# Optimization experiments

Measured on AMD Instinct MI355X. Metric: run time of the kernel, lower is better.

Reference implementation:

```python
import jax, jax.numpy as jnp
import numpy as np

EPS = 1e-5
N_NODES = 50000


def batchnorm(x, gamma, beta):
    # training-mode BatchNorm1d: batch mean, biased variance
    mean = jnp.mean(x, axis=0)
    var = jnp.mean(jnp.square(x - mean), axis=0)
    return (x - mean) * jax.lax.rsqrt(var + EPS) * gamma + beta


def setup_inputs() -> dict:
    key = jax.random.key(0)
    ks = jax.random.split(key, 8)
    N, E, D_IN, D_H, D_OUT = N_NODES, 800000, 128, 128, 128
    feat = jax.random.normal(ks[0], (N, D_IN), dtype=jnp.float32)
    w = jax.random.uniform(ks[1], (E,), dtype=jnp.float32)
    # xavier_uniform with relu gain for Q and W
    gain = float(np.sqrt(2.0))
    bq = gain * np.sqrt(6.0 / (D_IN + D_H))
    bw = gain * np.sqrt(6.0 / (D_IN + D_H + D_OUT))
    Q_w = jax.random.uniform(ks[2], (D_H, D_IN), minval=-bq, maxval=bq, dtype=jnp.float32)
    W_w = jax.random.uniform(ks[3], (D_OUT, D_IN + D_H), minval=-bw, maxval=bw, dtype=jnp.float32)
    Q_b = jnp.zeros((D_H,), jnp.float32)
    W_b = jnp.zeros((D_OUT,), jnp.float32)
    gamma2 = jnp.ones((D_OUT,), jnp.float32)
    beta2 = jnp.zeros((D_OUT,), jnp.float32)
    src = jax.random.randint(ks[4], (E,), 0, N, dtype=jnp.int32)
    dst = jax.random.randint(ks[5], (E,), 0, N, dtype=jnp.int32)
    return {"feat": feat, "w": w, "Q_w": Q_w, "Q_b": Q_b, "W_w": W_w,
            "W_b": W_b, "gamma2": gamma2, "beta2": beta2, "src": src, "dst": dst}


def reference(feat, w, Q_w, Q_b, W_w, W_b, gamma2, beta2, src, dst):
    N = feat.shape[0]
    # h = dropout(bnorm_two(relu(Q(feat))))  (dropout=0 -> identity; source reuses bnorm_two)
    h = batchnorm(jax.nn.relu(feat @ Q_w.T + Q_b), gamma2, beta2)  # [N, H]
    # weighted neighbor mean: sum_e w_e * h[src_e] scattered to dst, / sum_e w_e
    num = jax.ops.segment_sum(w[:, None] * h[src], dst, num_segments=N)  # [N, H]
    den = jax.ops.segment_sum(w, dst, num_segments=N)  # [N]
    has_msg = den[:, None] != 0
    agg = jnp.where(has_msg, num / jnp.where(has_msg, den[:, None], 1.0), h)
    rst = jnp.concatenate([feat, agg], axis=1) @ W_w.T + W_b  # [N, OUT]
    rst = batchnorm(jax.nn.relu(rst), gamma2, beta2)
    denom = jnp.linalg.norm(rst, axis=1, keepdims=True)
    return rst / jnp.where(denom == 0, 1.0, denom)
```

## Files before the change

### kernel.cpp

```cpp
#include <hip/hip_runtime.h>
#include <stdint.h>


#define BN_EPS 1e-5f
#define NSLOT 32

typedef __attribute__((ext_vector_type(8))) short bf16x8;
typedef __attribute__((ext_vector_type(4))) float f32x4;

static __device__ __forceinline__ unsigned short f2bf(float f) {
    uint32_t u = __builtin_bit_cast(uint32_t, f);
    u += 0x7fffu + ((u >> 16) & 1u);
    return (unsigned short)(u >> 16);
}
static __device__ __forceinline__ float bf_lo(uint32_t u) {
    return __builtin_bit_cast(float, u << 16);
}
static __device__ __forceinline__ float bf_hi(uint32_t u) {
    return __builtin_bit_cast(float, u & 0xffff0000u);
}

__global__ __launch_bounds__(256) void k_pre(
    const float* __restrict__ feat, unsigned short* __restrict__ featb, int nf,
    const int* __restrict__ dst, int* __restrict__ ccnt, int E, int CB)
{
    if ((int)blockIdx.x < CB) {
        int i = (blockIdx.x * 256 + threadIdx.x) * 4;
        if (i + 3 < nf) {
            float4 v = *(const float4*)(feat + i);
            ushort4 o;
            o.x = f2bf(v.x); o.y = f2bf(v.y); o.z = f2bf(v.z); o.w = f2bf(v.w);
            *(ushort4*)(featb + i) = o;
        } else {
            for (int j = i; j < nf; ++j) featb[j] = f2bf(feat[j]);
        }
    } else {
        __shared__ int hcnt[128];
        const int tid = threadIdx.x;
        if (tid < 128) hcnt[tid] = 0;
        __syncthreads();
        const int base_e = (blockIdx.x - CB) * 2048;
#pragma unroll
        for (int j = 0; j < 8; ++j) {
            int e = base_e + j * 256 + tid;
            if (e < E) atomicAdd(&hcnt[dst[e] >> 9], 1);
        }
        __syncthreads();
        if (tid < 128 && hcnt[tid] > 0) atomicAdd(&ccnt[tid], hcnt[tid]);
    }
}

__global__ __launch_bounds__(128) void k_coffs(
    const int* __restrict__ ccnt, int* __restrict__ coffs,
    int* __restrict__ gcur, int* __restrict__ offs, int N, int E)
{
    __shared__ int w0sum;
    const int t = threadIdx.x;
    const int lane = t & 63, wv = t >> 6;
    int v = ccnt[t];
    int incl = v;
#pragma unroll
    for (int o = 1; o < 64; o <<= 1) {
        int u = __shfl_up(incl, o, 64);
        if (lane >= o) incl += u;
    }
    if (wv == 0 && lane == 63) w0sum = incl;
    __syncthreads();
    int excl = incl - v + (wv ? w0sum : 0);
    coffs[t] = excl;
    gcur[t]  = excl;
    if (t == 127) { coffs[128] = excl + v; offs[N] = E; }
}

template<int K>
__global__ __launch_bounds__(256) void gemm_bn(
    const unsigned short* __restrict__ A_lo,
    const unsigned short* __restrict__ A_hi,
    const float* __restrict__ B,
    const float* __restrict__ bias,
    float* __restrict__ Y,
    double* __restrict__ sum, double* __restrict__ sumsq, int N)
{
    constexpr int SA = 72;
    __shared__ unsigned short As[64 * SA];
    __shared__ unsigned short Bs[128 * SA];
    __shared__ float bsum_s[128], bsq_s[128];

    const int tid  = threadIdx.x;
    const int lane = tid & 63;
    const int wv   = tid >> 6;
    const int wr   = wv >> 1;
    const int wc   = wv & 1;
    const int m15  = lane & 15;
    const int quad = lane >> 4;
    const int r0   = blockIdx.x * 64;

    if (tid < 128) { bsum_s[tid] = 0.f; bsq_s[tid] = 0.f; }

    f32x4 acc[2][4];
#pragma unroll
    for (int rt = 0; rt < 2; ++rt)
#pragma unroll
        for (int ct = 0; ct < 4; ++ct)
            acc[rt][ct] = (f32x4){0.f, 0.f, 0.f, 0.f};

    for (int kc = 0; kc < K; kc += 64) {
        const unsigned short* Ap = (kc < 128) ? A_lo : A_hi;
        const int koff = kc & 127;
#pragma unroll
        for (int i = 0; i < 2; ++i) {
            int idx = i * 256 + tid;
            int row = idx >> 3, seg = idx & 7;
            int gr  = r0 + row; if (gr >= N) gr = N - 1;
            uint4 v = *(const uint4*)(Ap + (size_t)gr * 128 + koff + seg * 8);
            *(uint4*)(As + row * SA + seg * 8) = v;
        }
#pragma unroll
        for (int i = 0; i < 8; ++i) {
            int idx = i * 256 + tid;
            int row = idx >> 4, seg = idx & 15;
            float4 v = *(const float4*)(B + (size_t)row * K + kc + seg * 4);
            ushort4 o;
            o.x = f2bf(v.x); o.y = f2bf(v.y); o.z = f2bf(v.z); o.w = f2bf(v.w);
            *(ushort4*)(Bs + row * SA + seg * 4) = o;
        }
        __syncthreads();

#pragma unroll
        for (int ks = 0; ks < 64; ks += 32) {
            bf16x8 af[2], bfr[4];
#pragma unroll
            for (int rt = 0; rt < 2; ++rt)
                af[rt] = *(const bf16x8*)(As + (wr * 32 + rt * 16 + m15) * SA + ks + quad * 8);
#pragma unroll
            for (int ct = 0; ct < 4; ++ct)
                bfr[ct] = *(const bf16x8*)(Bs + (wc * 64 + ct * 16 + m15) * SA + ks + quad * 8);
#pragma unroll
            for (int rt = 0; rt < 2; ++rt)
#pragma unroll
                for (int ct = 0; ct < 4; ++ct)
                    acc[rt][ct] = __builtin_amdgcn_mfma_f32_16x16x32_bf16(
                        af[rt], bfr[ct], acc[rt][ct], 0, 0, 0);
        }
        __syncthreads();
    }

#pragma unroll
    for (int ct = 0; ct < 4; ++ct) {
        int col = wc * 64 + ct * 16 + m15;
        float bz = bias[col];
        float s = 0.f, q = 0.f;
#pragma unroll
        for (int rt = 0; rt < 2; ++rt) {
#pragma unroll
            for (int reg = 0; reg < 4; ++reg) {
                int row = r0 + wr * 32 + rt * 16 + quad * 4 + reg;
                float v = fmaxf(acc[rt][ct][reg] + bz, 0.f);
                if (row < N) {
                    Y[(size_t)row * 128 + col] = v;
                } else {
                    v = 0.f;
                }
                s += v; q = fmaf(v, v, q);
            }
        }
        s += __shfl_xor(s, 16, 64); s += __shfl_xor(s, 32, 64);
        q += __shfl_xor(q, 16, 64); q += __shfl_xor(q, 32, 64);
        if (quad == 0) {
            atomicAdd(&bsum_s[col], s);
            atomicAdd(&bsq_s[col], q);
        }
    }
    __syncthreads();
    if (tid < 128) {
        const int slot = (blockIdx.x & (NSLOT - 1)) * 128;
        atomicAdd(&sum[slot + tid],   (double)bsum_s[tid]);
        atomicAdd(&sumsq[slot + tid], (double)bsq_s[tid]);
    }
}

__global__ __launch_bounds__(128) void bn_coef(
    const double* __restrict__ sum, const double* __restrict__ sumsq,
    const float* __restrict__ gamma, const float* __restrict__ beta,
    float* __restrict__ a, float* __restrict__ b, double invN)
{
    const int t = threadIdx.x;
    double ms = 0.0, qs = 0.0;
#pragma unroll
    for (int s = 0; s < NSLOT; ++s) {
        ms += sum[s * 128 + t];
        qs += sumsq[s * 128 + t];
    }
    float mean = (float)(ms * invN);
    float var  = (float)(qs * invN) - mean * mean;
    float sc = rsqrtf(var + BN_EPS) * gamma[t];
    a[t] = sc;
    b[t] = fmaf(-mean, sc, beta[t]);
}

__global__ __launch_bounds__(256) void apply_bn_bf16(
    const float* __restrict__ y,
    const float* __restrict__ a, const float* __restrict__ b,
    unsigned short* __restrict__ h, int n)
{
    int i = (blockIdx.x * 256 + threadIdx.x) * 4;
    if (i >= n) return;
    int c = i & 127;
    float4 v  = *(const float4*)(y + i);
    float4 av = *(const float4*)(a + c);
    float4 bv = *(const float4*)(b + c);
    ushort4 o;
    o.x = f2bf(fmaf(av.x, v.x, bv.x));
    o.y = f2bf(fmaf(av.y, v.y, bv.y));
    o.z = f2bf(fmaf(av.z, v.z, bv.z));
    o.w = f2bf(fmaf(av.w, v.w, bv.w));
    *(ushort4*)(h + i) = o;
}

__global__ __launch_bounds__(256) void k_bin(
    const int* __restrict__ src, const int* __restrict__ dst,
    const float* __restrict__ w, int* __restrict__ gcur,
    int4* __restrict__ tmp, int E)
{
    __shared__ int hcnt[128];
    __shared__ int hbase[128];
    const int tid = threadIdx.x;
    if (tid < 128) hcnt[tid] = 0;
    __syncthreads();

    int d8[8], s8[8], slot8[8];
    float w8[8];
#pragma unroll
    for (int j = 0; j < 8; ++j) {
        int e = blockIdx.x * 2048 + j * 256 + tid;
        if (e < E) {
            d8[j] = dst[e]; s8[j] = src[e]; w8[j] = w[e];
            slot8[j] = atomicAdd(&hcnt[d8[j] >> 9], 1);
        } else d8[j] = -1;
    }
    __syncthreads();
    if (tid < 128 && hcnt[tid] > 0)
        hbase[tid] = atomicAdd(&gcur[tid], hcnt[tid]);
    __syncthreads();
#pragma unroll
    for (int j = 0; j < 8; ++j) {
        if (d8[j] >= 0) {
            int pos = hbase[d8[j] >> 9] + slot8[j];
            tmp[pos] = make_int4(s8[j], __float_as_int(w8[j]), d8[j], 0);
        }
    }
}

__global__ __launch_bounds__(256) void k_refine(
    const int4* __restrict__ tmp, const int* __restrict__ coffs,
    int* __restrict__ offs, int2* __restrict__ epack, int N)
{
    __shared__ int hist[512];
    __shared__ int wpre[4];
    const int b    = blockIdx.x;
    const int d0   = b << 9;
    const int dlim = min(512, N - d0);
    const int tid  = threadIdx.x;
    const int lane = tid & 63, wv = tid >> 6;
    const int start = coffs[b];
    const int end   = coffs[b + 1];

    hist[tid] = 0; hist[tid + 256] = 0;
    __syncthreads();

    for (int p = start + tid; p < end; p += 256)
        atomicAdd(&hist[tmp[p].z - d0], 1);
    __syncthreads();

    int v0 = hist[2 * tid], v1 = hist[2 * tid + 1];
    int s = v0 + v1;
    int incl = s;
#pragma unroll
    for (int o = 1; o < 64; o <<= 1) {
        int t = __shfl_up(incl, o, 64);
        if (lane >= o) incl += t;
    }
    if (lane == 63) wpre[wv] = incl;
    __syncthreads();
    if (tid == 0) {
        int r = 0;
#pragma unroll
        for (int i = 0; i < 4; ++i) { int t = wpre[i]; wpre[i] = r; r += t; }
    }
    __syncthreads();
    int e0 = start + wpre[wv] + incl - s;
    if (2 * tid < dlim)     offs[d0 + 2 * tid]     = e0;
    if (2 * tid + 1 < dlim) offs[d0 + 2 * tid + 1] = e0 + v0;
    hist[2 * tid]     = e0;
    hist[2 * tid + 1] = e0 + v0;
    __syncthreads();

    for (int p = start + tid; p < end; p += 256) {
        int4 rec = tmp[p];
        int pos = atomicAdd(&hist[rec.z - d0], 1);
        epack[pos] = make_int2(rec.x, rec.y);
    }
}

__global__ __launch_bounds__(256) void gather_agg(
    const unsigned short* __restrict__ h,
    const int* __restrict__ offs, const int2* __restrict__ epack,
    unsigned short* __restrict__ aggb, int N)
{
    const int r    = (int)((blockIdx.x * 256u + threadIdx.x) >> 6);
    const int lane = threadIdx.x & 63;
    if (r >= N) return;
    int p = offs[r];
    const int end = offs[r + 1];
    float nx = 0.f, ny = 0.f, den = 0.f;
    for (; p + 3 < end; p += 4) {
        int2 e0 = epack[p],     e1 = epack[p + 1];
        int2 e2 = epack[p + 2], e3 = epack[p + 3];
        uint32_t u0 = *(const uint32_t*)(h + (size_t)e0.x * 128 + 2 * lane);
        uint32_t u1 = *(const uint32_t*)(h + (size_t)e1.x * 128 + 2 * lane);
        uint32_t u2 = *(const uint32_t*)(h + (size_t)e2.x * 128 + 2 * lane);
        uint32_t u3 = *(const uint32_t*)(h + (size_t)e3.x * 128 + 2 * lane);
        float w0 = __int_as_float(e0.y), w1 = __int_as_float(e1.y);
        float w2 = __int_as_float(e2.y), w3 = __int_as_float(e3.y);
        nx = fmaf(w0, bf_lo(u0), nx); ny = fmaf(w0, bf_hi(u0), ny);
        nx = fmaf(w1, bf_lo(u1), nx); ny = fmaf(w1, bf_hi(u1), ny);
        nx = fmaf(w2, bf_lo(u2), nx); ny = fmaf(w2, bf_hi(u2), ny);
        nx = fmaf(w3, bf_lo(u3), nx); ny = fmaf(w3, bf_hi(u3), ny);
        den += (w0 + w1) + (w2 + w3);
    }
    for (; p < end; ++p) {
        int2 e0 = epack[p];
        float w0 = __int_as_float(e0.y);
        uint32_t u0 = *(const uint32_t*)(h + (size_t)e0.x * 128 + 2 * lane);
        nx = fmaf(w0, bf_lo(u0), nx); ny = fmaf(w0, bf_hi(u0), ny);
        den += w0;
    }
    float2 outv;
    if (den != 0.f) {
        float inv = 1.f / den;
        outv.x = nx * inv; outv.y = ny * inv;
    } else {
        uint32_t u = *(const uint32_t*)(h + (size_t)r * 128 + 2 * lane);
        outv.x = bf_lo(u); outv.y = bf_hi(u);
    }
    ushort2 ao; ao.x = f2bf(outv.x); ao.y = f2bf(outv.y);
    *(ushort2*)&aggb[(size_t)r * 128 + 2 * lane] = ao;
}

__global__ __launch_bounds__(256) void finalize(
    const float* __restrict__ Y2,
    const float* __restrict__ a, const float* __restrict__ b,
    float* __restrict__ out, int N)
{
    __shared__ float sa[128], sb[128];
    const int t = threadIdx.x;
    if (t < 128) { sa[t] = a[t]; sb[t] = b[t]; }
    __syncthreads();
    const int row  = (int)((blockIdx.x * 256u + t) >> 6);
    const int lane = t & 63;
    if (row >= N) return;
    const size_t base = (size_t)row * 128;
    float v0 = fmaf(sa[lane],      Y2[base + lane],      sb[lane]);
    float v1 = fmaf(sa[lane + 64], Y2[base + lane + 64], sb[lane + 64]);
    float ss = fmaf(v0, v0, v1 * v1);
#pragma unroll
    for (int o = 32; o; o >>= 1) ss += __shfl_xor(ss, o, 64);
    float nrm = sqrtf(ss);
    float inv = (nrm == 0.f) ? 1.f : 1.f / nrm;
    out[base + lane]      = v0 * inv;
    out[base + lane + 64] = v1 * inv;
}

extern "C" void kernel_launch(void* const* d_in, const int* in_sizes, int n_in,
                              void* d_out, int out_size, void* d_ws, size_t ws_size,
                              hipStream_t stream)
{
    const float* feat   = (const float*)d_in[0];
    const float* w      = (const float*)d_in[1];
    const float* Q_w    = (const float*)d_in[2];
    const float* Q_b    = (const float*)d_in[3];
    const float* W_w    = (const float*)d_in[4];
    const float* W_b    = (const float*)d_in[5];
    const float* gamma2 = (const float*)d_in[6];
    const float* beta2  = (const float*)d_in[7];
    const int*   src    = (const int*)d_in[8];
    const int*   dst    = (const int*)d_in[9];

    const int N = in_sizes[0] / 128;
    const int E = in_sizes[1];

    float*          y1    = (float*)d_ws;
    unsigned short* featb = (unsigned short*)(y1 + (size_t)N * 128);
    unsigned short* aggb  = featb + (size_t)N * 128;
    unsigned short* h_bf  = aggb + (size_t)N * 128;
    int4*  tmp    = (int4*)(h_bf + (size_t)N * 128);
    int2*  epack  = (int2*)(tmp + E);
    int*   offs   = (int*)(epack + E);
    int*   coffs  = offs + (N + 1);
    int*   gcur   = coffs + 129;
    float* coefs  = (float*)(gcur + 128);
    float* a1 = coefs, *b1 = coefs + 128, *a2 = coefs + 256, *b2 = coefs + 384;
    uintptr_t sp  = ((uintptr_t)(coefs + 512) + 7) & ~(uintptr_t)7;
    double* stats = (double*)sp;
    double* sum1   = stats;
    double* sumsq1 = stats + NSLOT * 128;
    double* sum2   = stats + 2 * NSLOT * 128;
    double* sumsq2 = stats + 3 * NSLOT * 128;
    int*   ccnt   = (int*)(stats + 4 * NSLOT * 128);

    hipMemsetAsync(stats, 0,
                   4 * NSLOT * 128 * sizeof(double) + 128 * sizeof(int),
                   stream);

    const double invN = 1.0 / (double)N;
    const int gemm_blocks = (N + 63) / 64;
    const int NB = (N + 511) >> 9;
    const int CB = (N * 128 / 4 + 255) / 256;
    const int HB = (E + 2047) / 2048;

    k_pre<<<CB + HB, 256, 0, stream>>>(feat, featb, N * 128, dst, ccnt, E, CB);
    k_coffs<<<1, 128, 0, stream>>>(ccnt, coffs, gcur, offs, N, E);

    k_bin<<<HB, 256, 0, stream>>>(src, dst, w, gcur, tmp, E);
    k_refine<<<NB, 256, 0, stream>>>(tmp, coffs, offs, epack, N);

    gemm_bn<128><<<gemm_blocks, 256, 0, stream>>>(
        featb, featb, Q_w, Q_b, y1, sum1, sumsq1, N);
    bn_coef<<<1, 128, 0, stream>>>(sum1, sumsq1, gamma2, beta2, a1, b1, invN);
    apply_bn_bf16<<<(N * 128 + 1023) / 1024, 256, 0, stream>>>(
        y1, a1, b1, h_bf, N * 128);

    gather_agg<<<(N * 64 + 255) / 256, 256, 0, stream>>>(h_bf, offs, epack, aggb, N);

    gemm_bn<256><<<gemm_blocks, 256, 0, stream>>>(
        featb, aggb, W_w, W_b, y1 , sum2, sumsq2, N);
    bn_coef<<<1, 128, 0, stream>>>(sum2, sumsq2, gamma2, beta2, a2, b2, invN);
    finalize<<<(N * 64 + 255) / 256, 256, 0, stream>>>(
        y1, a2, b2, (float*)d_out, N);
}
```

Measured before the change: 254.3 us.

## Merge independent kernels into combined launches via block-index dispatch

Combines edge binning and the first GEMM+BN-stat pass into one launch, with blocks split by index range. It also combines CSR refinement with the BN-apply-to-bf16 pass. This removes two kernel launches and lets independent graph-preprocessing work run alongside dense work on the same device. The cost is that the union of shared memory and register use from both bodies now applies to every block, which may reduce occupancy.

```diff
diff --git a/kernel.cpp b/kernel.cpp
--- a/kernel.cpp
+++ b/kernel.cpp
@@ -73,7 +73,8 @@
 }
 
 template<int K>
-__global__ __launch_bounds__(256) void gemm_bn(
+static __device__ __forceinline__ void gemm_body(
+    int bid,
     const unsigned short* __restrict__ A_lo,
     const unsigned short* __restrict__ A_hi,
     const float* __restrict__ B,
@@ -93,7 +94,7 @@
     const int wc   = wv & 1;
     const int m15  = lane & 15;
     const int quad = lane >> 4;
-    const int r0   = blockIdx.x * 64;
+    const int r0   = bid * 64;
 
     if (tid < 128) { bsum_s[tid] = 0.f; bsq_s[tid] = 0.f; }
 
@@ -173,10 +174,60 @@
     }
     __syncthreads();
     if (tid < 128) {
-        const int slot = (blockIdx.x & (NSLOT - 1)) * 128;
+        const int slot = (bid & (NSLOT - 1)) * 128;
         atomicAdd(&sum[slot + tid],   (double)bsum_s[tid]);
         atomicAdd(&sumsq[slot + tid], (double)bsq_s[tid]);
     }
+}
+
+static __device__ __forceinline__ void bin_body(
+    int bid,
+    const int* __restrict__ src, const int* __restrict__ dst,
+    const float* __restrict__ w, int* __restrict__ gcur,
+    int4* __restrict__ tmp, int E)
+{
+    __shared__ int hcnt[128];
+    __shared__ int hbase[128];
+    const int tid = threadIdx.x;
+    if (tid < 128) hcnt[tid] = 0;
+    __syncthreads();
+
+    int d8[8], s8[8], slot8[8];
+    float w8[8];
+#pragma unroll
+    for (int j = 0; j < 8; ++j) {
+        int e = bid * 2048 + j * 256 + tid;
+        if (e < E) {
+            d8[j] = dst[e]; s8[j] = src[e]; w8[j] = w[e];
+            slot8[j] = atomicAdd(&hcnt[d8[j] >> 9], 1);
+        } else d8[j] = -1;
+    }
+    __syncthreads();
+    if (tid < 128 && hcnt[tid] > 0)
+        hbase[tid] = atomicAdd(&gcur[tid], hcnt[tid]);
+    __syncthreads();
+#pragma unroll
+    for (int j = 0; j < 8; ++j) {
+        if (d8[j] >= 0) {
+            int pos = hbase[d8[j] >> 9] + slot8[j];
+            tmp[pos] = make_int4(s8[j], __float_as_int(w8[j]), d8[j], 0);
+        }
+    }
+}
+
+__global__ __launch_bounds__(256) void k_bin_gemm(
+    const int* __restrict__ src, const int* __restrict__ dst,
+    const float* __restrict__ w, int* __restrict__ gcur,
+    int4* __restrict__ tmp, int E, int HB,
+    const unsigned short* __restrict__ featb,
+    const float* __restrict__ Qw, const float* __restrict__ Qb,
+    float* __restrict__ y1,
+    double* __restrict__ sum, double* __restrict__ sumsq, int N)
+{
+    if ((int)blockIdx.x < HB)
+        bin_body(blockIdx.x, src, dst, w, gcur, tmp, E);
+    else
+        gemm_body<128>(blockIdx.x - HB, featb, featb, Qw, Qb, y1, sum, sumsq, N);
 }
 
 __global__ __launch_bounds__(128) void bn_coef(
@@ -198,66 +249,13 @@
     b[t] = fmaf(-mean, sc, beta[t]);
 }
 
-__global__ __launch_bounds__(256) void apply_bn_bf16(
-    const float* __restrict__ y,
-    const float* __restrict__ a, const float* __restrict__ b,
-    unsigned short* __restrict__ h, int n)
-{
-    int i = (blockIdx.x * 256 + threadIdx.x) * 4;
-    if (i >= n) return;
-    int c = i & 127;
-    float4 v  = *(const float4*)(y + i);
-    float4 av = *(const float4*)(a + c);
-    float4 bv = *(const float4*)(b + c);
-    ushort4 o;
-    o.x = f2bf(fmaf(av.x, v.x, bv.x));
-    o.y = f2bf(fmaf(av.y, v.y, bv.y));
-    o.z = f2bf(fmaf(av.z, v.z, bv.z));
-    o.w = f2bf(fmaf(av.w, v.w, bv.w));
-    *(ushort4*)(h + i) = o;
-}
-
-__global__ __launch_bounds__(256) void k_bin(
-    const int* __restrict__ src, const int* __restrict__ dst,
-    const float* __restrict__ w, int* __restrict__ gcur,
-    int4* __restrict__ tmp, int E)
-{
-    __shared__ int hcnt[128];
-    __shared__ int hbase[128];
-    const int tid = threadIdx.x;
-    if (tid < 128) hcnt[tid] = 0;
-    __syncthreads();
-
-    int d8[8], s8[8], slot8[8];
-    float w8[8];
-#pragma unroll
-    for (int j = 0; j < 8; ++j) {
-        int e = blockIdx.x * 2048 + j * 256 + tid;
-        if (e < E) {
-            d8[j] = dst[e]; s8[j] = src[e]; w8[j] = w[e];
-            slot8[j] = atomicAdd(&hcnt[d8[j] >> 9], 1);
-        } else d8[j] = -1;
-    }
-    __syncthreads();
-    if (tid < 128 && hcnt[tid] > 0)
-        hbase[tid] = atomicAdd(&gcur[tid], hcnt[tid]);
-    __syncthreads();
-#pragma unroll
-    for (int j = 0; j < 8; ++j) {
-        if (d8[j] >= 0) {
-            int pos = hbase[d8[j] >> 9] + slot8[j];
-            tmp[pos] = make_int4(s8[j], __float_as_int(w8[j]), d8[j], 0);
-        }
-    }
-}
-
-__global__ __launch_bounds__(256) void k_refine(
+static __device__ __forceinline__ void refine_body(
+    int b,
     const int4* __restrict__ tmp, const int* __restrict__ coffs,
     int* __restrict__ offs, int2* __restrict__ epack, int N)
 {
     __shared__ int hist[512];
     __shared__ int wpre[4];
-    const int b    = blockIdx.x;
     const int d0   = b << 9;
     const int dlim = min(512, N - d0);
     const int tid  = threadIdx.x;
@@ -299,6 +297,31 @@
         int4 rec = tmp[p];
         int pos = atomicAdd(&hist[rec.z - d0], 1);
         epack[pos] = make_int2(rec.x, rec.y);
+    }
+}
+
+__global__ __launch_bounds__(256) void k_refine_apply(
+    const int4* __restrict__ tmp, const int* __restrict__ coffs,
+    int* __restrict__ offs, int2* __restrict__ epack, int N, int NB,
+    const float* __restrict__ y,
+    const float* __restrict__ a, const float* __restrict__ b,
+    unsigned short* __restrict__ h, int n)
+{
+    if ((int)blockIdx.x < NB) {
+        refine_body(blockIdx.x, tmp, coffs, offs, epack, N);
+    } else {
+        int i = ((blockIdx.x - NB) * 256 + threadIdx.x) * 4;
+        if (i >= n) return;
+        int c = i & 127;
+        float4 v  = *(const float4*)(y + i);
+        float4 av = *(const float4*)(a + c);
+        float4 bv = *(const float4*)(b + c);
+        ushort4 o;
+        o.x = f2bf(fmaf(av.x, v.x, bv.x));
+        o.y = f2bf(fmaf(av.y, v.y, bv.y));
+        o.z = f2bf(fmaf(av.z, v.z, bv.z));
+        o.w = f2bf(fmaf(av.w, v.w, bv.w));
+        *(ushort4*)(h + i) = o;
     }
 }
 
@@ -347,6 +370,17 @@
     *(ushort2*)&aggb[(size_t)r * 128 + 2 * lane] = ao;
 }
 
+__global__ __launch_bounds__(256) void gemm_bn2(
+    const unsigned short* __restrict__ A_lo,
+    const unsigned short* __restrict__ A_hi,
+    const float* __restrict__ B,
+    const float* __restrict__ bias,
+    float* __restrict__ Y,
+    double* __restrict__ sum, double* __restrict__ sumsq, int N)
+{
+    gemm_body<256>(blockIdx.x, A_lo, A_hi, B, bias, Y, sum, sumsq, N);
+}
+
 __global__ __launch_bounds__(256) void finalize(
     const float* __restrict__ Y2,
     const float* __restrict__ a, const float* __restrict__ b,
@@ -413,26 +447,27 @@
                    stream);
 
     const double invN = 1.0 / (double)N;
-    const int gemm_blocks = (N + 63) / 64;
+    const int GB = (N + 63) / 64;
     const int NB = (N + 511) >> 9;
     const int CB = (N * 128 / 4 + 255) / 256;
     const int HB = (E + 2047) / 2048;
+    const int AB = (N * 128 / 4 + 255) / 256;
 
     k_pre<<<CB + HB, 256, 0, stream>>>(feat, featb, N * 128, dst, ccnt, E, CB);
     k_coffs<<<1, 128, 0, stream>>>(ccnt, coffs, gcur, offs, N, E);
 
-    k_bin<<<HB, 256, 0, stream>>>(src, dst, w, gcur, tmp, E);
-    k_refine<<<NB, 256, 0, stream>>>(tmp, coffs, offs, epack, N);
-
-    gemm_bn<128><<<gemm_blocks, 256, 0, stream>>>(
-        featb, featb, Q_w, Q_b, y1, sum1, sumsq1, N);
+    k_bin_gemm<<<HB + GB, 256, 0, stream>>>(
+        src, dst, w, gcur, tmp, E, HB,
+        featb, Q_w, Q_b, y1, sum1, sumsq1, N);
     bn_coef<<<1, 128, 0, stream>>>(sum1, sumsq1, gamma2, beta2, a1, b1, invN);
-    apply_bn_bf16<<<(N * 128 + 1023) / 1024, 256, 0, stream>>>(
+
+    k_refine_apply<<<NB + AB, 256, 0, stream>>>(
+        tmp, coffs, offs, epack, N, NB,
         y1, a1, b1, h_bf, N * 128);
 
     gather_agg<<<(N * 64 + 255) / 256, 256, 0, stream>>>(h_bf, offs, epack, aggb, N);
 
-    gemm_bn<256><<<gemm_blocks, 256, 0, stream>>>(
+    gemm_bn2<<<GB, 256, 0, stream>>>(
         featb, aggb, W_w, W_b, y1 , sum2, sumsq2, N);
     bn_coef<<<1, 128, 0, stream>>>(sum2, sumsq2, gamma2, beta2, a2, b2, invN);
     finalize<<<(N * 64 + 255) / 256, 256, 0, stream>>>(
```

After: 245.3 us. -3.6%, faster.

## Fuse all stages into one persistent cooperative kernel with grid syncs

Applied to the files above, without the earlier changes.

Replaces the chain of about a dozen kernel launches and the memset with a single cooperative persistent kernel. Stages are separated by grid.sync(), blocks loop over work units, and shared memory is a union reused across stages. Independent stages are merged into the same phase: edge binning runs alongside the first GEMM, and the refine step alongside BN apply. This removes launch gaps and idle tails between stages. In exchange it adds grid-wide barrier costs, caps the grid at the occupancy-derived block count, and keeps a multi-kernel fallback.

```diff
diff --git a/kernel.cpp b/kernel.cpp
--- a/kernel.cpp
+++ b/kernel.cpp
@@ -1,5 +1,8 @@
 #include <hip/hip_runtime.h>
+#include <hip/hip_cooperative_groups.h>
 #include <stdint.h>
+
+namespace cg = cooperative_groups;
 
 
 #define BN_EPS 1e-5f
@@ -20,60 +23,119 @@
     return __builtin_bit_cast(float, u & 0xffff0000u);
 }
 
-__global__ __launch_bounds__(256) void k_pre(
-    const float* __restrict__ feat, unsigned short* __restrict__ featb, int nf,
-    const int* __restrict__ dst, int* __restrict__ ccnt, int E, int CB)
-{
-    if ((int)blockIdx.x < CB) {
-        int i = (blockIdx.x * 256 + threadIdx.x) * 4;
-        if (i + 3 < nf) {
-            float4 v = *(const float4*)(feat + i);
-            ushort4 o;
-            o.x = f2bf(v.x); o.y = f2bf(v.y); o.z = f2bf(v.z); o.w = f2bf(v.w);
-            *(ushort4*)(featb + i) = o;
-        } else {
-            for (int j = i; j < nf; ++j) featb[j] = f2bf(feat[j]);
-        }
+union Smem {
+    struct { unsigned short As[64 * 72]; unsigned short Bs[128 * 72];
+             float bs[128]; float bq[128]; } g;
+    struct { int hcnt[128]; int hbase[128]; } b;
+    struct { int hist[512]; int wpre[4]; } r;
+    struct { float sa[128]; float sb[128]; } f;
+};
+
+struct P {
+    const float *feat, *w, *Qw, *Qb, *Ww, *Wb, *gamma2, *beta2;
+    const int *src, *dst;
+    float* out;
+    float* y1; unsigned short *featb, *aggb, *h_bf;
+    int4* tmp; int2* epack; int *offs, *coffs, *gcur;
+    float* coefs; double* stats; int* ccnt;
+    int N, E, CB, HB, GB, NB, AB, ZI;
+    double invN;
+};
+
+static __device__ __forceinline__ void cast_body(
+    int u, const float* __restrict__ feat, unsigned short* __restrict__ featb, int nf)
+{
+    int i = (u * 256 + threadIdx.x) * 4;
+    if (i + 3 < nf) {
+        float4 v = *(const float4*)(feat + i);
+        ushort4 o;
+        o.x = f2bf(v.x); o.y = f2bf(v.y); o.z = f2bf(v.z); o.w = f2bf(v.w);
+        *(ushort4*)(featb + i) = o;
     } else {
-        __shared__ int hcnt[128];
-        const int tid = threadIdx.x;
-        if (tid < 128) hcnt[tid] = 0;
-        __syncthreads();
-        const int base_e = (blockIdx.x - CB) * 2048;
-#pragma unroll
-        for (int j = 0; j < 8; ++j) {
-            int e = base_e + j * 256 + tid;
-            if (e < E) atomicAdd(&hcnt[dst[e] >> 9], 1);
-        }
-        __syncthreads();
-        if (tid < 128 && hcnt[tid] > 0) atomicAdd(&ccnt[tid], hcnt[tid]);
-    }
-}
-
-__global__ __launch_bounds__(128) void k_coffs(
-    const int* __restrict__ ccnt, int* __restrict__ coffs,
+        for (int j = i; j < nf; ++j) featb[j] = f2bf(feat[j]);
+    }
+}
+
+static __device__ __forceinline__ void hist_body(
+    Smem& sm, int u, const int* __restrict__ dst, int* __restrict__ ccnt, int E)
+{
+    const int tid = threadIdx.x;
+    __syncthreads();
+    if (tid < 128) sm.b.hcnt[tid] = 0;
+    __syncthreads();
+    const int base_e = u * 2048;
+#pragma unroll
+    for (int j = 0; j < 8; ++j) {
+        int e = base_e + j * 256 + tid;
+        if (e < E) atomicAdd(&sm.b.hcnt[dst[e] >> 9], 1);
+    }
+    __syncthreads();
+    if (tid < 128 && sm.b.hcnt[tid] > 0) atomicAdd(&ccnt[tid], sm.b.hcnt[tid]);
+}
+
+static __device__ __forceinline__ void coffs_body(
+    Smem& sm, const int* __restrict__ ccnt, int* __restrict__ coffs,
     int* __restrict__ gcur, int* __restrict__ offs, int N, int E)
 {
-    __shared__ int w0sum;
     const int t = threadIdx.x;
-    const int lane = t & 63, wv = t >> 6;
-    int v = ccnt[t];
-    int incl = v;
-#pragma unroll
-    for (int o = 1; o < 64; o <<= 1) {
-        int u = __shfl_up(incl, o, 64);
-        if (lane >= o) incl += u;
-    }
-    if (wv == 0 && lane == 63) w0sum = incl;
-    __syncthreads();
-    int excl = incl - v + (wv ? w0sum : 0);
-    coffs[t] = excl;
-    gcur[t]  = excl;
-    if (t == 127) { coffs[128] = excl + v; offs[N] = E; }
+    __syncthreads();
+    int v = 0, incl = 0;
+    if (t < 128) {
+        v = ccnt[t];
+        incl = v;
+#pragma unroll
+        for (int o = 1; o < 64; o <<= 1) {
+            int u = __shfl_up(incl, o, 64);
+            if ((t & 63) >= o) incl += u;
+        }
+        if (t == 63) sm.r.wpre[0] = incl;
+    }
+    __syncthreads();
+    if (t < 128) {
+        int excl = incl - v + ((t >= 64) ? sm.r.wpre[0] : 0);
+        coffs[t] = excl;
+        gcur[t]  = excl;
+        if (t == 127) { coffs[128] = excl + v; offs[N] = E; }
+    }
+}
+
+static __device__ __forceinline__ void bin_body(
+    Smem& sm, int bid,
+    const int* __restrict__ src, const int* __restrict__ dst,
+    const float* __restrict__ w, int* __restrict__ gcur,
+    int4* __restrict__ tmp, int E)
+{
+    const int tid = threadIdx.x;
+    __syncthreads();
+    if (tid < 128) sm.b.hcnt[tid] = 0;
+    __syncthreads();
+
+    int d8[8], s8[8], slot8[8];
+    float w8[8];
+#pragma unroll
+    for (int j = 0; j < 8; ++j) {
+        int e = bid * 2048 + j * 256 + tid;
+        if (e < E) {
+            d8[j] = dst[e]; s8[j] = src[e]; w8[j] = w[e];
+            slot8[j] = atomicAdd(&sm.b.hcnt[d8[j] >> 9], 1);
+        } else d8[j] = -1;
+    }
+    __syncthreads();
+    if (tid < 128 && sm.b.hcnt[tid] > 0)
+        sm.b.hbase[tid] = atomicAdd(&gcur[tid], sm.b.hcnt[tid]);
+    __syncthreads();
+#pragma unroll
+    for (int j = 0; j < 8; ++j) {
+        if (d8[j] >= 0) {
+            int pos = sm.b.hbase[d8[j] >> 9] + slot8[j];
+            tmp[pos] = make_int4(s8[j], __float_as_int(w8[j]), d8[j], 0);
+        }
+    }
 }
 
 template<int K>
-__global__ __launch_bounds__(256) void gemm_bn(
+static __device__ __forceinline__ void gemm_body(
+    Smem& sm, int bid,
     const unsigned short* __restrict__ A_lo,
     const unsigned short* __restrict__ A_hi,
     const float* __restrict__ B,
@@ -82,10 +144,6 @@
     double* __restrict__ sum, double* __restrict__ sumsq, int N)
 {
     constexpr int SA = 72;
-    __shared__ unsigned short As[64 * SA];
-    __shared__ unsigned short Bs[128 * SA];
-    __shared__ float bsum_s[128], bsq_s[128];
-
     const int tid  = threadIdx.x;
     const int lane = tid & 63;
     const int wv   = tid >> 6;
@@ -93,9 +151,10 @@
     const int wc   = wv & 1;
     const int m15  = lane & 15;
     const int quad = lane >> 4;
-    const int r0   = blockIdx.x * 64;
-
-    if (tid < 128) { bsum_s[tid] = 0.f; bsq_s[tid] = 0.f; }
+    const int r0   = bid * 64;
+
+    __syncthreads();
+    if (tid < 128) { sm.g.bs[tid] = 0.f; sm.g.bq[tid] = 0.f; }
 
     f32x4 acc[2][4];
 #pragma unroll
@@ -113,7 +172,7 @@
             int row = idx >> 3, seg = idx & 7;
             int gr  = r0 + row; if (gr >= N) gr = N - 1;
             uint4 v = *(const uint4*)(Ap + (size_t)gr * 128 + koff + seg * 8);
-            *(uint4*)(As + row * SA + seg * 8) = v;
+            *(uint4*)(sm.g.As + row * SA + seg * 8) = v;
         }
 #pragma unroll
         for (int i = 0; i < 8; ++i) {
@@ -122,7 +181,7 @@
             float4 v = *(const float4*)(B + (size_t)row * K + kc + seg * 4);
             ushort4 o;
             o.x = f2bf(v.x); o.y = f2bf(v.y); o.z = f2bf(v.z); o.w = f2bf(v.w);
-            *(ushort4*)(Bs + row * SA + seg * 4) = o;
+            *(ushort4*)(sm.g.Bs + row * SA + seg * 4) = o;
         }
         __syncthreads();
 
@@ -131,10 +190,10 @@
             bf16x8 af[2], bfr[4];
 #pragma unroll
             for (int rt = 0; rt < 2; ++rt)
-                af[rt] = *(const bf16x8*)(As + (wr * 32 + rt * 16 + m15) * SA + ks + quad * 8);
+                af[rt] = *(const bf16x8*)(sm.g.As + (wr * 32 + rt * 16 + m15) * SA + ks + quad * 8);
 #pragma unroll
             for (int ct = 0; ct < 4; ++ct)
-                bfr[ct] = *(const bf16x8*)(Bs + (wc * 64 + ct * 16 + m15) * SA + ks + quad * 8);
+                bfr[ct] = *(const bf16x8*)(sm.g.Bs + (wc * 64 + ct * 16 + m15) * SA + ks + quad * 8);
 #pragma unroll
             for (int rt = 0; rt < 2; ++rt)
 #pragma unroll
@@ -167,24 +226,25 @@
         s += __shfl_xor(s, 16, 64); s += __shfl_xor(s, 32, 64);
         q += __shfl_xor(q, 16, 64); q += __shfl_xor(q, 32, 64);
         if (quad == 0) {
-            atomicAdd(&bsum_s[col], s);
-            atomicAdd(&bsq_s[col], q);
+            atomicAdd(&sm.g.bs[col], s);
+            atomicAdd(&sm.g.bq[col], q);
         }
     }
     __syncthreads();
     if (tid < 128) {
-        const int slot = (blockIdx.x & (NSLOT - 1)) * 128;
-        atomicAdd(&sum[slot + tid],   (double)bsum_s[tid]);
-        atomicAdd(&sumsq[slot + tid], (double)bsq_s[tid]);
-    }
-}
-
-__global__ __launch_bounds__(128) void bn_coef(
+        const int slot = (bid & (NSLOT - 1)) * 128;
+        atomicAdd(&sum[slot + tid],   (double)sm.g.bs[tid]);
+        atomicAdd(&sumsq[slot + tid], (double)sm.g.bq[tid]);
+    }
+}
+
+static __device__ __forceinline__ void bn_coef_body(
     const double* __restrict__ sum, const double* __restrict__ sumsq,
     const float* __restrict__ gamma, const float* __restrict__ beta,
     float* __restrict__ a, float* __restrict__ b, double invN)
 {
     const int t = threadIdx.x;
+    if (t >= 128) return;
     double ms = 0.0, qs = 0.0;
 #pragma unroll
     for (int s = 0; s < NSLOT; ++s) {
@@ -198,12 +258,12 @@
     b[t] = fmaf(-mean, sc, beta[t]);
 }
 
-__global__ __launch_bounds__(256) void apply_bn_bf16(
-    const float* __restrict__ y,
+static __device__ __forceinline__ void apply_body(
+    int u, const float* __restrict__ y,
     const float* __restrict__ a, const float* __restrict__ b,
     unsigned short* __restrict__ h, int n)
 {
-    int i = (blockIdx.x * 256 + threadIdx.x) * 4;
+    int i = (u * 256 + threadIdx.x) * 4;
     if (i >= n) return;
     int c = i & 127;
     float4 v  = *(const float4*)(y + i);
@@ -217,47 +277,11 @@
     *(ushort4*)(h + i) = o;
 }
 
-__global__ __launch_bounds__(256) void k_bin(
-    const int* __restrict__ src, const int* __restrict__ dst,
-    const float* __restrict__ w, int* __restrict__ gcur,
-    int4* __restrict__ tmp, int E)
-{
-    __shared__ int hcnt[128];
-    __shared__ int hbase[128];
-    const int tid = threadIdx.x;
-    if (tid < 128) hcnt[tid] = 0;
-    __syncthreads();
-
-    int d8[8], s8[8], slot8[8];
-    float w8[8];
-#pragma unroll
-    for (int j = 0; j < 8; ++j) {
-        int e = blockIdx.x * 2048 + j * 256 + tid;
-        if (e < E) {
-            d8[j] = dst[e]; s8[j] = src[e]; w8[j] = w[e];
-            slot8[j] = atomicAdd(&hcnt[d8[j] >> 9], 1);
-        } else d8[j] = -1;
-    }
-    __syncthreads();
-    if (tid < 128 && hcnt[tid] > 0)
-        hbase[tid] = atomicAdd(&gcur[tid], hcnt[tid]);
-    __syncthreads();
-#pragma unroll
-    for (int j = 0; j < 8; ++j) {
-        if (d8[j] >= 0) {
-            int pos = hbase[d8[j] >> 9] + slot8[j];
-            tmp[pos] = make_int4(s8[j], __float_as_int(w8[j]), d8[j], 0);
-        }
-    }
-}
-
-__global__ __launch_bounds__(256) void k_refine(
+static __device__ __forceinline__ void refine_body(
+    Smem& sm, int b,
     const int4* __restrict__ tmp, const int* __restrict__ coffs,
     int* __restrict__ offs, int2* __restrict__ epack, int N)
 {
-    __shared__ int hist[512];
-    __shared__ int wpre[4];
-    const int b    = blockIdx.x;
     const int d0   = b << 9;
     const int dlim = min(512, N - d0);
     const int tid  = threadIdx.x;
@@ -265,14 +289,15 @@
     const int start = coffs[b];
     const int end   = coffs[b + 1];
 
-    hist[tid] = 0; hist[tid + 256] = 0;
+    __syncthreads();
+    sm.r.hist[tid] = 0; sm.r.hist[tid + 256] = 0;
     __syncthreads();
 
     for (int p = start + tid; p < end; p += 256)
-        atomicAdd(&hist[tmp[p].z - d0], 1);
-    __syncthreads();
-
-    int v0 = hist[2 * tid], v1 = hist[2 * tid + 1];
+        atomicAdd(&sm.r.hist[tmp[p].z - d0], 1);
+    __syncthreads();
+
+    int v0 = sm.r.hist[2 * tid], v1 = sm.r.hist[2 * tid + 1];
     int s = v0 + v1;
     int incl = s;
 #pragma unroll
@@ -280,36 +305,35 @@
         int t = __shfl_up(incl, o, 64);
         if (lane >= o) incl += t;
     }
-    if (lane == 63) wpre[wv] = incl;
+    if (lane == 63) sm.r.wpre[wv] = incl;
     __syncthreads();
     if (tid == 0) {
         int r = 0;
 #pragma unroll
-        for (int i = 0; i < 4; ++i) { int t = wpre[i]; wpre[i] = r; r += t; }
-    }
-    __syncthreads();
-    int e0 = start + wpre[wv] + incl - s;
+        for (int i = 0; i < 4; ++i) { int t = sm.r.wpre[i]; sm.r.wpre[i] = r; r += t; }
+    }
+    __syncthreads();
+    int e0 = start + sm.r.wpre[wv] + incl - s;
     if (2 * tid < dlim)     offs[d0 + 2 * tid]     = e0;
     if (2 * tid + 1 < dlim) offs[d0 + 2 * tid + 1] = e0 + v0;
-    hist[2 * tid]     = e0;
-    hist[2 * tid + 1] = e0 + v0;
+    __syncthreads();
+    sm.r.hist[2 * tid]     = e0;
+    sm.r.hist[2 * tid + 1] = e0 + v0;
     __syncthreads();
 
     for (int p = start + tid; p < end; p += 256) {
         int4 rec = tmp[p];
-        int pos = atomicAdd(&hist[rec.z - d0], 1);
+        int pos = atomicAdd(&sm.r.hist[rec.z - d0], 1);
         epack[pos] = make_int2(rec.x, rec.y);
     }
 }
 
-__global__ __launch_bounds__(256) void gather_agg(
+static __device__ __forceinline__ void gather_row(
+    int r, int lane,
     const unsigned short* __restrict__ h,
     const int* __restrict__ offs, const int2* __restrict__ epack,
-    unsigned short* __restrict__ aggb, int N)
-{
-    const int r    = (int)((blockIdx.x * 256u + threadIdx.x) >> 6);
-    const int lane = threadIdx.x & 63;
-    if (r >= N) return;
+    unsigned short* __restrict__ aggb)
+{
     int p = offs[r];
     const int end = offs[r + 1];
     float nx = 0.f, ny = 0.f, den = 0.f;
@@ -347,19 +371,11 @@
     *(ushort2*)&aggb[(size_t)r * 128 + 2 * lane] = ao;
 }
 
-__global__ __launch_bounds__(256) void finalize(
-    const float* __restrict__ Y2,
-    const float* __restrict__ a, const float* __restrict__ b,
-    float* __restrict__ out, int N)
-{
-    __shared__ float sa[128], sb[128];
-    const int t = threadIdx.x;
-    if (t < 128) { sa[t] = a[t]; sb[t] = b[t]; }
-    __syncthreads();
-    const int row  = (int)((blockIdx.x * 256u + t) >> 6);
-    const int lane = t & 63;
-    if (row >= N) return;
-    const size_t base = (size_t)row * 128;
+static __device__ __forceinline__ void final_row(
+    int r, int lane, const float* __restrict__ Y2,
+    const float* sa, const float* sb, float* __restrict__ out)
+{
+    const size_t base = (size_t)r * 128;
     float v0 = fmaf(sa[lane],      Y2[base + lane],      sb[lane]);
     float v1 = fmaf(sa[lane + 64], Y2[base + lane + 64], sb[lane + 64]);
     float ss = fmaf(v0, v0, v1 * v1);
@@ -371,21 +387,144 @@
     out[base + lane + 64] = v1 * inv;
 }
 
+__global__ __launch_bounds__(256) void mega(P p)
+{
+    cg::grid_group grid = cg::this_grid();
+    __shared__ Smem sm;
+    const int tid  = threadIdx.x;
+    const int nb   = gridDim.x;
+    const int wv   = tid >> 6, lane = tid & 63;
+
+    {
+        int* z = (int*)p.stats;
+        for (int i = blockIdx.x * 256 + tid; i < p.ZI; i += nb * 256) z[i] = 0;
+    }
+    grid.sync();
+
+    for (int u = blockIdx.x; u < p.CB + p.HB; u += nb) {
+        if (u < p.CB) cast_body(u, p.feat, p.featb, p.N * 128);
+        else          hist_body(sm, u - p.CB, p.dst, p.ccnt, p.E);
+    }
+    grid.sync();
+
+    if (blockIdx.x == 0) coffs_body(sm, p.ccnt, p.coffs, p.gcur, p.offs, p.N, p.E);
+    grid.sync();
+
+    for (int u = blockIdx.x; u < p.HB + p.GB; u += nb) {
+        if (u < p.HB) bin_body(sm, u, p.src, p.dst, p.w, p.gcur, p.tmp, p.E);
+        else          gemm_body<128>(sm, u - p.HB, p.featb, p.featb, p.Qw, p.Qb,
+                                     p.y1, p.stats, p.stats + NSLOT * 128, p.N);
+    }
+    grid.sync();
+
+    if (blockIdx.x == 0)
+        bn_coef_body(p.stats, p.stats + NSLOT * 128, p.gamma2, p.beta2,
+                     p.coefs, p.coefs + 128, p.invN);
+    grid.sync();
+
+    for (int u = blockIdx.x; u < p.NB + p.AB; u += nb) {
+        if (u < p.NB) refine_body(sm, u, p.tmp, p.coffs, p.offs, p.epack, p.N);
+        else          apply_body(u - p.NB, p.y1, p.coefs, p.coefs + 128,
+                                 p.h_bf, p.N * 128);
+    }
+    grid.sync();
+
+    {
+        const int UN = (p.N + 3) >> 2;
+        for (int u = blockIdx.x; u < UN; u += nb) {
+            int r = u * 4 + wv;
+            if (r < p.N) gather_row(r, lane, p.h_bf, p.offs, p.epack, p.aggb);
+        }
+    }
+    grid.sync();
+
+    for (int u = blockIdx.x; u < p.GB; u += nb)
+        gemm_body<256>(sm, u, p.featb, p.aggb, p.Ww, p.Wb, p.y1,
+                       p.stats + 2 * NSLOT * 128, p.stats + 3 * NSLOT * 128, p.N);
+    grid.sync();
+
+    if (blockIdx.x == 0)
+        bn_coef_body(p.stats + 2 * NSLOT * 128, p.stats + 3 * NSLOT * 128,
+                     p.gamma2, p.beta2, p.coefs + 256, p.coefs + 384, p.invN);
+    grid.sync();
+
+    {
+        __syncthreads();
+        if (tid < 128) { sm.f.sa[tid] = p.coefs[256 + tid];
+                         sm.f.sb[tid] = p.coefs[384 + tid]; }
+        __syncthreads();
+        const int UN = (p.N + 3) >> 2;
+        for (int u = blockIdx.x; u < UN; u += nb) {
+            int r = u * 4 + wv;
+            if (r < p.N) final_row(r, lane, p.y1, sm.f.sa, sm.f.sb, p.out);
+        }
+    }
+}
+
+__global__ __launch_bounds__(256) void fk_pre(P p)
+{
+    __shared__ Smem sm;
+    if ((int)blockIdx.x < p.CB) cast_body(blockIdx.x, p.feat, p.featb, p.N * 128);
+    else hist_body(sm, blockIdx.x - p.CB, p.dst, p.ccnt, p.E);
+}
+__global__ __launch_bounds__(256) void fk_coffs(P p)
+{
+    __shared__ Smem sm;
+    coffs_body(sm, p.ccnt, p.coffs, p.gcur, p.offs, p.N, p.E);
+}
+__global__ __launch_bounds__(256) void fk_bin_gemm(P p)
+{
+    __shared__ Smem sm;
+    if ((int)blockIdx.x < p.HB)
+        bin_body(sm, blockIdx.x, p.src, p.dst, p.w, p.gcur, p.tmp, p.E);
+    else
+        gemm_body<128>(sm, blockIdx.x - p.HB, p.featb, p.featb, p.Qw, p.Qb,
+                       p.y1, p.stats, p.stats + NSLOT * 128, p.N);
+}
+__global__ __launch_bounds__(128) void fk_bn1(P p)
+{
+    bn_coef_body(p.stats, p.stats + NSLOT * 128, p.gamma2, p.beta2,
+                 p.coefs, p.coefs + 128, p.invN);
+}
+__global__ __launch_bounds__(256) void fk_refine_apply(P p)
+{
+    __shared__ Smem sm;
+    if ((int)blockIdx.x < p.NB)
+        refine_body(sm, blockIdx.x, p.tmp, p.coffs, p.offs, p.epack, p.N);
+    else
+        apply_body(blockIdx.x - p.NB, p.y1, p.coefs, p.coefs + 128,
+                   p.h_bf, p.N * 128);
+}
+__global__ __launch_bounds__(256) void fk_gather(P p)
+{
+    const int r = (int)((blockIdx.x * 256u + threadIdx.x) >> 6);
+    if (r < p.N) gather_row(r, threadIdx.x & 63, p.h_bf, p.offs, p.epack, p.aggb);
+}
+__global__ __launch_bounds__(256) void fk_gemm2(P p)
+{
+    __shared__ Smem sm;
+    gemm_body<256>(sm, blockIdx.x, p.featb, p.aggb, p.Ww, p.Wb, p.y1,
+                   p.stats + 2 * NSLOT * 128, p.stats + 3 * NSLOT * 128, p.N);
+}
+__global__ __launch_bounds__(128) void fk_bn2(P p)
+{
+    bn_coef_body(p.stats + 2 * NSLOT * 128, p.stats + 3 * NSLOT * 128,
+                 p.gamma2, p.beta2, p.coefs + 256, p.coefs + 384, p.invN);
+}
+__global__ __launch_bounds__(256) void fk_finalize(P p)
+{
+    __shared__ float sa[128], sb[128];
+    const int t = threadIdx.x;
+    if (t < 128) { sa[t] = p.coefs[256 + t]; sb[t] = p.coefs[384 + t]; }
+    __syncthreads();
+    const int r = (int)((blockIdx.x * 256u + t) >> 6);
+    if (r < p.N) final_row(r, t & 63, p.y1, sa, sb, p.out);
+}
+
 extern "C" void kernel_launch(void* const* d_in, const int* in_sizes, int n_in,
                               void* d_out, int out_size, void* d_ws, size_t ws_size,
                               hipStream_t stream)
 {
-    const float* feat   = (const float*)d_in[0];
-    const float* w      = (const float*)d_in[1];
-    const float* Q_w    = (const float*)d_in[2];
-    const float* Q_b    = (const float*)d_in[3];
-    const float* W_w    = (const float*)d_in[4];
-    const float* W_b    = (const float*)d_in[5];
-    const float* gamma2 = (const float*)d_in[6];
-    const float* beta2  = (const float*)d_in[7];
-    const int*   src    = (const int*)d_in[8];
-    const int*   dst    = (const int*)d_in[9];
-
     const int N = in_sizes[0] / 128;
     const int E = in_sizes[1];
 
@@ -399,42 +538,48 @@
     int*   coffs  = offs + (N + 1);
     int*   gcur   = coffs + 129;
     float* coefs  = (float*)(gcur + 128);
-    float* a1 = coefs, *b1 = coefs + 128, *a2 = coefs + 256, *b2 = coefs + 384;
     uintptr_t sp  = ((uintptr_t)(coefs + 512) + 7) & ~(uintptr_t)7;
     double* stats = (double*)sp;
-    double* sum1   = stats;
-    double* sumsq1 = stats + NSLOT * 128;
-    double* sum2   = stats + 2 * NSLOT * 128;
-    double* sumsq2 = stats + 3 * NSLOT * 128;
-    int*   ccnt   = (int*)(stats + 4 * NSLOT * 128);
-
-    hipMemsetAsync(stats, 0,
-                   4 * NSLOT * 128 * sizeof(double) + 128 * sizeof(int),
-                   stream);
-
-    const double invN = 1.0 / (double)N;
-    const int gemm_blocks = (N + 63) / 64;
-    const int NB = (N + 511) >> 9;
-    const int CB = (N * 128 / 4 + 255) / 256;
-    const int HB = (E + 2047) / 2048;
-
-    k_pre<<<CB + HB, 256, 0, stream>>>(feat, featb, N * 128, dst, ccnt, E, CB);
-    k_coffs<<<1, 128, 0, stream>>>(ccnt, coffs, gcur, offs, N, E);
-
-    k_bin<<<HB, 256, 0, stream>>>(src, dst, w, gcur, tmp, E);
-    k_refine<<<NB, 256, 0, stream>>>(tmp, coffs, offs, epack, N);
-
-    gemm_bn<128><<<gemm_blocks, 256, 0, stream>>>(
-        featb, featb, Q_w, Q_b, y1, sum1, sumsq1, N);
-    bn_coef<<<1, 128, 0, stream>>>(sum1, sumsq1, gamma2, beta2, a1, b1, invN);
-    apply_bn_bf16<<<(N * 128 + 1023) / 1024, 256, 0, stream>>>(
-        y1, a1, b1, h_bf, N * 128);
-
-    gather_agg<<<(N * 64 + 255) / 256, 256, 0, stream>>>(h_bf, offs, epack, aggb, N);
-
-    gemm_bn<256><<<gemm_blocks, 256, 0, stream>>>(
-        featb, aggb, W_w, W_b, y1 , sum2, sumsq2, N);
-    bn_coef<<<1, 128, 0, stream>>>(sum2, sumsq2, gamma2, beta2, a2, b2, invN);
-    finalize<<<(N * 64 + 255) / 256, 256, 0, stream>>>(
-        y1, a2, b2, (float*)d_out, N);
-}
+    int*    ccnt  = (int*)(stats + 4 * NSLOT * 128);
+
+    P p;
+    p.feat = (const float*)d_in[0]; p.w = (const float*)d_in[1];
+    p.Qw = (const float*)d_in[2];   p.Qb = (const float*)d_in[3];
+    p.Ww = (const float*)d_in[4];   p.Wb = (const float*)d_in[5];
+    p.gamma2 = (const float*)d_in[6]; p.beta2 = (const float*)d_in[7];
+    p.src = (const int*)d_in[8];    p.dst = (const int*)d_in[9];
+    p.out = (float*)d_out;
+    p.y1 = y1; p.featb = featb; p.aggb = aggb; p.h_bf = h_bf;
+    p.tmp = tmp; p.epack = epack; p.offs = offs; p.coffs = coffs; p.gcur = gcur;
+    p.coefs = coefs; p.stats = stats; p.ccnt = ccnt;
+    p.N = N; p.E = E;
+    p.CB = (N * 128 / 4 + 255) / 256;
+    p.HB = (E + 2047) / 2048;
+    p.GB = (N + 63) / 64;
+    p.NB = (N + 511) >> 9;
+    p.AB = (N * 128 / 4 + 255) / 256;
+    p.ZI = 4 * NSLOT * 128 * 2 + 128;
+    p.invN = 1.0 / (double)N;
+
+    int bpc = 0;
+    hipError_t oe = hipOccupancyMaxActiveBlocksPerMultiprocessor(&bpc, mega, 256, 0);
+    hipError_t le = hipErrorUnknown;
+    if (oe == hipSuccess && bpc >= 1) {
+        int G = bpc * 256;
+        if (G > 2048) G = 2048;
+        void* kargs[] = { (void*)&p };
+        le = hipLaunchCooperativeKernel(mega, dim3(G), dim3(256), kargs, 0, stream);
+    }
+    if (le != hipSuccess) {
+        hipMemsetAsync(stats, 0, (size_t)p.ZI * sizeof(int), stream);
+        fk_pre<<<p.CB + p.HB, 256, 0, stream>>>(p);
+        fk_coffs<<<1, 256, 0, stream>>>(p);
+        fk_bin_gemm<<<p.HB + p.GB, 256, 0, stream>>>(p);
+        fk_bn1<<<1, 128, 0, stream>>>(p);
+        fk_refine_apply<<<p.NB + p.AB, 256, 0, stream>>>(p);
+        fk_gather<<<(N * 64 + 255) / 256, 256, 0, stream>>>(p);
+        fk_gemm2<<<p.GB, 256, 0, stream>>>(p);
+        fk_bn2<<<1, 128, 0, stream>>>(p);
+        fk_finalize<<<(N * 64 + 255) / 256, 256, 0, stream>>>(p);
+    }
+}
```

Result: slower. 694.2 us (+173.0%).
